# Optimization experiments

Measured on AMD Instinct MI355X. Metric: run time of the kernel, lower is better.

The kernel has to match this reference:

```python
import jax, jax.numpy as jnp
import numpy as np

N, E, C = 50000, 300000, 256  # nodes, edges, hidden size


def setup_inputs() -> dict:
    key = jax.random.key(0)
    ks = jax.random.split(key, 12)
    s = 0.05  # param init scale
    return {
        "x": jax.random.normal(ks[0], (N, C), dtype=jnp.float32),
        "edge_index": jax.random.randint(ks[1], (2, E), 0, N, dtype=jnp.int32),
        # GATConv layer 1 (heads=1): shared lin weight, att_src/att_dst vectors, bias
        "W1": jax.random.normal(ks[2], (C, C), dtype=jnp.float32) * s,
        "a1_src": jax.random.normal(ks[3], (C,), dtype=jnp.float32) * s,
        "a1_dst": jax.random.normal(ks[4], (C,), dtype=jnp.float32) * s,
        "b1": jnp.zeros((C,), dtype=jnp.float32),
        # GATConv layer 2
        "W2": jax.random.normal(ks[5], (C, C), dtype=jnp.float32) * s,
        "a2_src": jax.random.normal(ks[6], (C,), dtype=jnp.float32) * s,
        "a2_dst": jax.random.normal(ks[7], (C,), dtype=jnp.float32) * s,
        "b2": jnp.zeros((C,), dtype=jnp.float32),
        # Final Linear (torch convention: W [out, in], y = x @ W.T + b)
        "Wl": jax.random.normal(ks[8], (C, C), dtype=jnp.float32) * s,
        "bl": jnp.zeros((C,), dtype=jnp.float32),
    }


def _gat_conv(x, src, dst, W, a_src, a_dst, b):
    # PyG GATConv, heads=1, negative_slope=0.2, self-loops already appended.
    h = x @ W                                  # [N, C]
    alpha_src = h @ a_src                      # [N]
    alpha_dst = h @ a_dst                      # [N]
    e = jax.nn.leaky_relu(alpha_src[src] + alpha_dst[dst], 0.2)   # [E']
    # numerically stable softmax over incoming edges of each destination node
    m = jax.ops.segment_max(e, dst, num_segments=N)               # [N]
    ex = jnp.exp(e - m[dst])
    den = jax.ops.segment_sum(ex, dst, num_segments=N)            # [N]
    w = ex / den[dst]                                              # [E']
    out = jax.ops.segment_sum(h[src] * w[:, None], dst, num_segments=N)  # [N, C]
    return out + b


def reference(x, edge_index, W1, a1_src, a1_dst, b1, W2, a2_src, a2_dst, b2, Wl, bl):
    # add_self_loops (done inside each GATConv in PyG; appending once to the
    # input edge list is equivalent since both convs see the same edges)
    loops = jnp.arange(N, dtype=edge_index.dtype)
    ei = jnp.concatenate([edge_index, jnp.stack([loops, loops])], axis=1)
    src, dst = ei[0], ei[1]
    x = jax.nn.relu(_gat_conv(x, src, dst, W1, a1_src, a1_dst, b1))
    x = jax.nn.relu(_gat_conv(x, src, dst, W2, a2_src, a2_dst, b2))
    return x @ Wl.T + bl
```

## Files before the change

kernel.cpp:

```cpp
#include <hip/hip_runtime.h>

#define NN 50000
#define EE 300000
#define ET (EE + NN)
#define CD 256
#define PAD_M 50176
#define NB 196

typedef unsigned short ushortT;
typedef short bf16x8 __attribute__((ext_vector_type(8)));
typedef float f32x4 __attribute__((ext_vector_type(4)));

__device__ __forceinline__ ushortT f2b(float f) {
    unsigned u = __builtin_bit_cast(unsigned, f);
    unsigned r = (u + 0x7FFFu + ((u >> 16) & 1u)) >> 16;
    return (ushortT)r;
}
__device__ __forceinline__ float b2f(ushortT b) {
    return __builtin_bit_cast(float, ((unsigned)b) << 16);
}


__global__ __launch_bounds__(256) void wvec_kernel(
    const float* __restrict__ W1, const float* __restrict__ a1s,
    const float* __restrict__ a1d, const float* __restrict__ W2,
    const float* __restrict__ a2s, const float* __restrict__ a2d,
    float* __restrict__ w1s, float* __restrict__ w1d,
    float* __restrict__ w2s, float* __restrict__ w2d) {
    int b = blockIdx.x;
    const float* W = (b < 64) ? W1 : W2;
    const float* vs = (b < 64) ? a1s : a2s;
    const float* vd = (b < 64) ? a1d : a2d;
    float* os = (b < 64) ? w1s : w2s;
    float* od = (b < 64) ? w1d : w2d;
    int r = (b & 63) * 4 + (threadIdx.x >> 6);
    int lane = threadIdx.x & 63;
    float4 wv = *(const float4*)(W + (size_t)r * CD + lane * 4);
    float4 s4 = *(const float4*)(vs + lane * 4);
    float4 d4 = *(const float4*)(vd + lane * 4);
    float ss = wv.x * s4.x + wv.y * s4.y + wv.z * s4.z + wv.w * s4.w;
    float dd = wv.x * d4.x + wv.y * d4.y + wv.z * d4.z + wv.w * d4.w;
#pragma unroll
    for (int off = 1; off < 64; off <<= 1) {
        ss += __shfl_xor(ss, off);
        dd += __shfl_xor(dd, off);
    }
    if (lane == 0) {
        os[r] = ss;
        od[r] = dd;
    }
}

#define PREP_X 12500
#define PREP_W1 12564
#define PREP_W2 12628
#define PREP_WL 12692
#define PREP_END 12888

__global__ __launch_bounds__(256) void prep_kernel(
    const float* __restrict__ x, const float* __restrict__ W1,
    const float* __restrict__ W2, const float* __restrict__ Wl,
    ushortT* __restrict__ B0, ushortT* __restrict__ W1t,
    ushortT* __restrict__ W2t, ushortT* __restrict__ Wlt,
    int* __restrict__ deg, const float* __restrict__ w1s,
    const float* __restrict__ w1d, float* __restrict__ as1,
    float* __restrict__ ad1) {
    __shared__ float t[32][33];
    int b = blockIdx.x, tidx = threadIdx.x;
    if (b < PREP_X) {
        int node = b * 4 + (tidx >> 6);
        int lane = tidx & 63;
        float4 v = *(const float4*)(x + (size_t)node * CD + lane * 4);
        ushort4 o;
        o.x = f2b(v.x); o.y = f2b(v.y); o.z = f2b(v.z); o.w = f2b(v.w);
        *(ushort4*)(B0 + (size_t)node * CD + lane * 4) = o;
        float4 s4 = *(const float4*)(w1s + lane * 4);
        float4 d4 = *(const float4*)(w1d + lane * 4);
        float ss = v.x * s4.x + v.y * s4.y + v.z * s4.z + v.w * s4.w;
        float dd = v.x * d4.x + v.y * d4.y + v.z * d4.z + v.w * d4.w;
#pragma unroll
        for (int off = 1; off < 64; off <<= 1) {
            ss += __shfl_xor(ss, off);
            dd += __shfl_xor(dd, off);
        }
        if (lane == 0) {
            as1[node] = ss;
            ad1[node] = dd;
        }
    } else if (b < PREP_W2) {
        const float* W = (b < PREP_W1) ? W1 : W2;
        ushortT* Bt = (b < PREP_W1) ? W1t : W2t;
        int rel = b - ((b < PREP_W1) ? PREP_X : PREP_W1);
        int bx = (rel & 7) * 32;
        int by = (rel >> 3) * 32;
        int xx = tidx & 31, yy = tidx >> 5;
        for (int y = yy; y < 32; y += 8) t[y][xx] = W[(size_t)(bx + y) * CD + by + xx];
        __syncthreads();
        for (int y = yy; y < 32; y += 8)
            Bt[(size_t)(by + y) * CD + bx + xx] = f2b(t[xx][y]);
    } else if (b < PREP_WL) {
        int id = (b - PREP_W2) * 256 + tidx;
        float4 v = *(const float4*)(Wl + (size_t)id * 4);
        ushort4 o;
        o.x = f2b(v.x); o.y = f2b(v.y); o.z = f2b(v.z); o.w = f2b(v.w);
        *(ushort4*)(Wlt + (size_t)id * 4) = o;
    } else {
        int i = (b - PREP_WL) * 256 + tidx;
        if (i < NN) deg[i] = 1;
    }
}


__global__ void count_deg_kernel(const int* __restrict__ ei, int* __restrict__ deg) {
    int i = blockIdx.x * blockDim.x + threadIdx.x;
    if (i < EE) atomicAdd(&deg[ei[EE + i]], 1);
}

__global__ __launch_bounds__(256) void scan_part(const int* __restrict__ deg,
                                                 int* __restrict__ bsum) {
    int i = blockIdx.x * 256 + threadIdx.x;
    int v = (i < NN) ? deg[i] : 0;
#pragma unroll
    for (int off = 32; off > 0; off >>= 1) v += __shfl_down(v, off);
    __shared__ int w[4];
    if ((threadIdx.x & 63) == 0) w[threadIdx.x >> 6] = v;
    __syncthreads();
    if (threadIdx.x == 0) bsum[blockIdx.x] = w[0] + w[1] + w[2] + w[3];
}

__global__ __launch_bounds__(256) void scan_fill(const int* __restrict__ deg,
                                                 const int* __restrict__ bsum,
                                                 int* __restrict__ row_start,
                                                 int* __restrict__ fill_pos) {
    __shared__ int s[256];
    int t = threadIdx.x;
    int bv = (t < NB) ? bsum[t] : 0;
    s[t] = bv;
    __syncthreads();
    for (int off = 1; off < 256; off <<= 1) {
        int x = s[t];
        int y = (t >= off) ? s[t - off] : 0;
        __syncthreads();
        s[t] = x + y;
        __syncthreads();
    }
    int boff = s[blockIdx.x] - bsum[blockIdx.x];
    __syncthreads();
    int i = blockIdx.x * 256 + t;
    int v = (i < NN) ? deg[i] : 0;
    s[t] = v;
    __syncthreads();
    for (int off = 1; off < 256; off <<= 1) {
        int x = s[t];
        int y = (t >= off) ? s[t - off] : 0;
        __syncthreads();
        s[t] = x + y;
        __syncthreads();
    }
    int excl = s[t] - v + boff;
    if (i < NN) {
        row_start[i] = excl;
        fill_pos[i] = excl;
    }
    if (blockIdx.x == 0 && t == 0) row_start[NN] = ET;
}

__global__ void fill_csr_kernel(const int* __restrict__ ei, int* __restrict__ fill_pos,
                                int* __restrict__ srcs) {
    int i = blockIdx.x * blockDim.x + threadIdx.x;
    if (i < EE) {
        int s = ei[i];
        int d = ei[EE + i];
        int p = atomicAdd(&fill_pos[d], 1);
        srcs[p] = s;
    } else if (i < ET) {
        int n = i - EE;
        int p = atomicAdd(&fill_pos[n], 1);
        srcs[p] = n;
    }
}


template <int OUTF32>
__global__ __launch_bounds__(256, 4) void gemm_mfma(const ushortT* __restrict__ A,
                                                    const ushortT* __restrict__ Bt,
                                                    const float* __restrict__ bias,
                                                    float* __restrict__ outF,
                                                    ushortT* __restrict__ outB,
                                                    int M) {
    __shared__ ushortT Bs[64 * 256];
    int tid = threadIdx.x;
    int wave = tid >> 6, lane = tid & 63;
    int wm = wave * 32;
    int id = blockIdx.x;
    int bm = (id >> 2) * 128, bn = (id & 3) * 64;
    int l15 = lane & 15, quad = lane >> 4;

#pragma unroll
    for (int p = 0; p < 8; ++p) {
        int c = p * 256 + tid;
        int slot = c >> 5;
        int piece = c & 31;
        int col = (slot & 15) * 4 + (slot >> 4);
        int spiece = piece ^ (slot & 31);
        const ushortT* gb = Bt + (size_t)(bn + col) * CD + spiece * 8;
        __builtin_amdgcn_global_load_lds(
            (const __attribute__((address_space(1))) void*)gb,
            (__attribute__((address_space(3))) void*)(Bs + (size_t)(p * 256 + wave * 64) * 8),
            16, 0, 0);
    }

    bf16x8 a[2][8];
#pragma unroll
    for (int kk = 0; kk < 8; ++kk)
#pragma unroll
        for (int i = 0; i < 2; ++i)
            a[i][kk] = *(const bf16x8*)(A + (size_t)(bm + wm + i * 16 + l15) * CD + kk * 32 + quad * 8);

    __syncthreads();

    f32x4 acc[2][4] = {};

#pragma unroll
    for (int kk = 0; kk < 8; ++kk) {
        bf16x8 b[4];
        int kc = kk * 4 + quad;
#pragma unroll
        for (int j = 0; j < 4; ++j) {
            int slot = j * 16 + l15;
            b[j] = *(const bf16x8*)(Bs + (size_t)slot * 256 + (size_t)(kc ^ (slot & 31)) * 8);
        }
#pragma unroll
        for (int i = 0; i < 2; ++i)
#pragma unroll
            for (int j = 0; j < 4; ++j)
                acc[i][j] = __builtin_amdgcn_mfma_f32_16x16x32_bf16(a[i][kk], b[j], acc[i][j], 0, 0, 0);
    }

    int colb = bn + l15 * 4;
#pragma unroll
    for (int i = 0; i < 2; ++i) {
#pragma unroll
        for (int r = 0; r < 4; ++r) {
            int row = bm + wm + i * 16 + quad * 4 + r;
            if (OUTF32) {
                if (row < M) {
                    float4 bv = *(const float4*)(bias + colb);
                    float4 v;
                    v.x = acc[i][0][r] + bv.x;
                    v.y = acc[i][1][r] + bv.y;
                    v.z = acc[i][2][r] + bv.z;
                    v.w = acc[i][3][r] + bv.w;
                    *(float4*)(outF + (size_t)row * CD + colb) = v;
                }
            } else {
                ushort4 o;
                o.x = f2b(acc[i][0][r]);
                o.y = f2b(acc[i][1][r]);
                o.z = f2b(acc[i][2][r]);
                o.w = f2b(acc[i][3][r]);
                *(ushort4*)(outB + (size_t)row * CD + colb) = o;
            }
        }
    }
}


__device__ __forceinline__ float lrelu02(float x) { return x > 0.f ? x : 0.2f * x; }

template <int ALPHA2>
__global__ __launch_bounds__(256) void gat_agg(const ushortT* __restrict__ h,
                                               const float* __restrict__ as_,
                                               const float* __restrict__ ad_,
                                               const int* __restrict__ row_start,
                                               const int* __restrict__ srcs,
                                               const float* __restrict__ bias,
                                               ushortT* __restrict__ out,
                                               const float* __restrict__ w2s,
                                               const float* __restrict__ w2d,
                                               float* __restrict__ as_n,
                                               float* __restrict__ ad_n) {
    int node = blockIdx.x * 8 + (threadIdx.x >> 5);
    int hl = threadIdx.x & 31;
    if (node >= NN) return;
    int rs = row_start[node];
    int re = row_start[node + 1];
    int deg = re - rs;
    float adst = ad_[node];

    float acc[8] = {0.f, 0.f, 0.f, 0.f, 0.f, 0.f, 0.f, 0.f};

    int maxdeg = max(deg, __shfl_xor(deg, 32));

    if (maxdeg <= 32) {
        int s_lane = srcs[rs + ((hl < deg) ? hl : 0)];
        float e = (hl < deg) ? lrelu02(as_[s_lane] + adst) : -1e30f;
        float m = e;
#pragma unroll
        for (int off = 1; off < 32; off <<= 1) m = fmaxf(m, __shfl_xor(m, off));
        float ex = (hl < deg) ? __expf(e - m) : 0.f;
        float den = ex;
#pragma unroll
        for (int off = 1; off < 32; off <<= 1) den += __shfl_xor(den, off);
        float wl = ex / den;

        for (int kk = 0; kk < maxdeg; kk += 8) {
            int s[8];
            float w[8];
#pragma unroll
            for (int t = 0; t < 8; ++t) {
                int idx = kk + t;
                int ii = (idx < deg) ? idx : 0;
                int sv = __shfl(s_lane, ii, 32);
                float wv = __shfl(wl, ii, 32);
                s[t] = sv;
                w[t] = (idx < deg) ? wv : 0.f;
            }
            bf16x8 hv[8];
#pragma unroll
            for (int t = 0; t < 8; ++t)
                hv[t] = *(const bf16x8*)(h + (size_t)s[t] * CD + hl * 8);
#pragma unroll
            for (int t = 0; t < 8; ++t) {
#pragma unroll
                for (int c = 0; c < 8; ++c)
                    acc[c] += w[t] * b2f((ushortT)hv[t][c]);
            }
        }
    } else {
        float m = -1e30f;
        for (int k = rs + hl; k < re; k += 32) {
            float e = lrelu02(as_[srcs[k]] + adst);
            m = fmaxf(m, e);
        }
#pragma unroll
        for (int off = 1; off < 32; off <<= 1) m = fmaxf(m, __shfl_xor(m, off));
        float den = 0.f;
        for (int k = rs + hl; k < re; k += 32) {
            float e = lrelu02(as_[srcs[k]] + adst);
            den += __expf(e - m);
        }
#pragma unroll
        for (int off = 1; off < 32; off <<= 1) den += __shfl_xor(den, off);
        float inv_den = 1.f / den;
        for (int k = rs; k < re; ++k) {
            int sv = srcs[k];
            float e = lrelu02(as_[sv] + adst);
            float wv = __expf(e - m) * inv_den;
            bf16x8 hv = *(const bf16x8*)(h + (size_t)sv * CD + hl * 8);
#pragma unroll
            for (int c = 0; c < 8; ++c)
                acc[c] += wv * b2f((ushortT)hv[c]);
        }
    }

    float4 bv0 = *(const float4*)(bias + hl * 8);
    float4 bv1 = *(const float4*)(bias + hl * 8 + 4);
    float r[8];
    r[0] = fmaxf(acc[0] + bv0.x, 0.f);
    r[1] = fmaxf(acc[1] + bv0.y, 0.f);
    r[2] = fmaxf(acc[2] + bv0.z, 0.f);
    r[3] = fmaxf(acc[3] + bv0.w, 0.f);
    r[4] = fmaxf(acc[4] + bv1.x, 0.f);
    r[5] = fmaxf(acc[5] + bv1.y, 0.f);
    r[6] = fmaxf(acc[6] + bv1.z, 0.f);
    r[7] = fmaxf(acc[7] + bv1.w, 0.f);
    bf16x8 o;
#pragma unroll
    for (int c = 0; c < 8; ++c) o[c] = (short)f2b(r[c]);
    *(bf16x8*)(out + (size_t)node * CD + hl * 8) = o;

    if (ALPHA2) {
        float4 s0 = *(const float4*)(w2s + hl * 8);
        float4 s1 = *(const float4*)(w2s + hl * 8 + 4);
        float4 d0 = *(const float4*)(w2d + hl * 8);
        float4 d1 = *(const float4*)(w2d + hl * 8 + 4);
        float ss = r[0] * s0.x + r[1] * s0.y + r[2] * s0.z + r[3] * s0.w +
                   r[4] * s1.x + r[5] * s1.y + r[6] * s1.z + r[7] * s1.w;
        float dd = r[0] * d0.x + r[1] * d0.y + r[2] * d0.z + r[3] * d0.w +
                   r[4] * d1.x + r[5] * d1.y + r[6] * d1.z + r[7] * d1.w;
#pragma unroll
        for (int off = 1; off < 32; off <<= 1) {
            ss += __shfl_xor(ss, off);
            dd += __shfl_xor(dd, off);
        }
        if (hl == 0) {
            as_n[node] = ss;
            ad_n[node] = dd;
        }
    }
}


extern "C" void kernel_launch(void* const* d_in, const int* in_sizes, int n_in,
                              void* d_out, int out_size, void* d_ws, size_t ws_size,
                              hipStream_t stream) {
    const float* x = (const float*)d_in[0];
    const int* ei = (const int*)d_in[1];
    const float* W1 = (const float*)d_in[2];
    const float* a1s = (const float*)d_in[3];
    const float* a1d = (const float*)d_in[4];
    const float* b1 = (const float*)d_in[5];
    const float* W2 = (const float*)d_in[6];
    const float* a2s = (const float*)d_in[7];
    const float* a2d = (const float*)d_in[8];
    const float* b2 = (const float*)d_in[9];
    const float* Wl = (const float*)d_in[10];
    const float* bl = (const float*)d_in[11];
    float* out = (float*)d_out;

    char* w = (char*)d_ws;
    ushortT* B0 = (ushortT*)w; w += (size_t)PAD_M * CD * 2;
    ushortT* B1 = (ushortT*)w; w += (size_t)PAD_M * CD * 2;
    ushortT* B2 = (ushortT*)w; w += (size_t)PAD_M * CD * 2;
    ushortT* W1t = (ushortT*)w; w += (size_t)CD * CD * 2;
    ushortT* W2t = (ushortT*)w; w += (size_t)CD * CD * 2;
    ushortT* Wlt = (ushortT*)w; w += (size_t)CD * CD * 2;
    float* as1 = (float*)w; w += (size_t)NN * 4;
    float* ad1 = (float*)w; w += (size_t)NN * 4;
    float* as2 = (float*)w; w += (size_t)NN * 4;
    float* ad2 = (float*)w; w += (size_t)NN * 4;
    float* w1s = (float*)w; w += CD * 4;
    float* w1d = (float*)w; w += CD * 4;
    float* w2s = (float*)w; w += CD * 4;
    float* w2d = (float*)w; w += CD * 4;
    int* deg = (int*)w; w += (size_t)NN * 4;
    int* fill_pos = (int*)w; w += (size_t)NN * 4;
    int* srcs = (int*)w; w += (size_t)ET * 4;
    int* bsum = (int*)w; w += 1024;
    int* row_start = (int*)w; w += (size_t)(NN + 1) * 4;

    wvec_kernel<<<128, 256, 0, stream>>>(W1, a1s, a1d, W2, a2s, a2d,
                                         w1s, w1d, w2s, w2d);

    prep_kernel<<<PREP_END, 256, 0, stream>>>(x, W1, W2, Wl, B0, W1t, W2t, Wlt,
                                              deg, w1s, w1d, as1, ad1);

    count_deg_kernel<<<(EE + 255) / 256, 256, 0, stream>>>(ei, deg);
    scan_part<<<NB, 256, 0, stream>>>(deg, bsum);
    scan_fill<<<NB, 256, 0, stream>>>(deg, bsum, row_start, fill_pos);
    fill_csr_kernel<<<(ET + 255) / 256, 256, 0, stream>>>(ei, fill_pos, srcs);

    int ggrid = (PAD_M / 128) * 4;
    int nagg_blocks = (NN + 7) / 8;

    gemm_mfma<0><<<ggrid, 256, 0, stream>>>(B0, W1t, nullptr, nullptr, B1, NN);
    gat_agg<1><<<nagg_blocks, 256, 0, stream>>>(B1, as1, ad1, row_start, srcs,
                                                b1, B2, w2s, w2d, as2, ad2);

    gemm_mfma<0><<<ggrid, 256, 0, stream>>>(B2, W2t, nullptr, nullptr, B1, NN);
    gat_agg<0><<<nagg_blocks, 256, 0, stream>>>(B1, as2, ad2, row_start, srcs,
                                                b2, B0, nullptr, nullptr,
                                                nullptr, nullptr);

    gemm_mfma<1><<<ggrid, 256, 0, stream>>>(B0, Wlt, bl, out, nullptr, NN);
}
```

Measured before the change: 290.1 us.

## Fuse fp32-to-bf16 conversion and layer-1 attention logits into first GEMM

The separate prep pass that converted x to bf16 and computed the layer-1 alpha_src/alpha_dst dot products is removed. A new GEMM kernel reads fp32 x directly, converts it to bf16 in registers, and computes the attention logits in the column-block-0 tiles. This avoids writing and re-reading a bf16 copy of x. The cost is that each GEMM tile now reads fp32 A, and since there are four column blocks, x is read four times in fp32. The aggregation kernel also issues the first 8 neighbor row gathers before the softmax reductions so that memory latency overlaps the shuffle math.

After: 297.4 us. 2.5% more time.

```diff
diff --git a/kernel.cpp b/kernel.cpp
--- a/kernel.cpp
+++ b/kernel.cpp
@@ -51,46 +51,22 @@
     }
 }
 
-#define PREP_X 12500
-#define PREP_W1 12564
-#define PREP_W2 12628
-#define PREP_WL 12692
-#define PREP_END 12888
+#define PREP_W1 64
+#define PREP_W2 128
+#define PREP_WL 192
+#define PREP_END 388
 
 __global__ __launch_bounds__(256) void prep_kernel(
-    const float* __restrict__ x, const float* __restrict__ W1,
-    const float* __restrict__ W2, const float* __restrict__ Wl,
-    ushortT* __restrict__ B0, ushortT* __restrict__ W1t,
+    const float* __restrict__ W1, const float* __restrict__ W2,
+    const float* __restrict__ Wl, ushortT* __restrict__ W1t,
     ushortT* __restrict__ W2t, ushortT* __restrict__ Wlt,
-    int* __restrict__ deg, const float* __restrict__ w1s,
-    const float* __restrict__ w1d, float* __restrict__ as1,
-    float* __restrict__ ad1) {
+    int* __restrict__ deg) {
     __shared__ float t[32][33];
     int b = blockIdx.x, tidx = threadIdx.x;
-    if (b < PREP_X) {
-        int node = b * 4 + (tidx >> 6);
-        int lane = tidx & 63;
-        float4 v = *(const float4*)(x + (size_t)node * CD + lane * 4);
-        ushort4 o;
-        o.x = f2b(v.x); o.y = f2b(v.y); o.z = f2b(v.z); o.w = f2b(v.w);
-        *(ushort4*)(B0 + (size_t)node * CD + lane * 4) = o;
-        float4 s4 = *(const float4*)(w1s + lane * 4);
-        float4 d4 = *(const float4*)(w1d + lane * 4);
-        float ss = v.x * s4.x + v.y * s4.y + v.z * s4.z + v.w * s4.w;
-        float dd = v.x * d4.x + v.y * d4.y + v.z * d4.z + v.w * d4.w;
-#pragma unroll
-        for (int off = 1; off < 64; off <<= 1) {
-            ss += __shfl_xor(ss, off);
-            dd += __shfl_xor(dd, off);
-        }
-        if (lane == 0) {
-            as1[node] = ss;
-            ad1[node] = dd;
-        }
-    } else if (b < PREP_W2) {
+    if (b < PREP_W2) {
         const float* W = (b < PREP_W1) ? W1 : W2;
         ushortT* Bt = (b < PREP_W1) ? W1t : W2t;
-        int rel = b - ((b < PREP_W1) ? PREP_X : PREP_W1);
+        int rel = b - ((b < PREP_W1) ? 0 : PREP_W1);
         int bx = (rel & 7) * 32;
         int by = (rel >> 3) * 32;
         int xx = tidx & 31, yy = tidx >> 5;
@@ -266,6 +242,126 @@
 }
 
 
+__global__ __launch_bounds__(256, 2) void gemm_mfma_x(
+    const float* __restrict__ A, const ushortT* __restrict__ Bt,
+    ushortT* __restrict__ outB, const float* __restrict__ w1s,
+    const float* __restrict__ w1d, float* __restrict__ as1,
+    float* __restrict__ ad1) {
+    __shared__ ushortT Bs[64 * 256];
+    int tid = threadIdx.x;
+    int wave = tid >> 6, lane = tid & 63;
+    int wm = wave * 32;
+    int id = blockIdx.x;
+    int bm = (id >> 2) * 128, bn = (id & 3) * 64;
+    int l15 = lane & 15, quad = lane >> 4;
+
+#pragma unroll
+    for (int p = 0; p < 8; ++p) {
+        int c = p * 256 + tid;
+        int slot = c >> 5;
+        int piece = c & 31;
+        int col = (slot & 15) * 4 + (slot >> 4);
+        int spiece = piece ^ (slot & 31);
+        const ushortT* gb = Bt + (size_t)(bn + col) * CD + spiece * 8;
+        __builtin_amdgcn_global_load_lds(
+            (const __attribute__((address_space(1))) void*)gb,
+            (__attribute__((address_space(3))) void*)(Bs + (size_t)(p * 256 + wave * 64) * 8),
+            16, 0, 0);
+    }
+
+    int r0 = bm + wm + l15;
+    int r1 = r0 + 16;
+    const float* A0 = A + (size_t)((r0 < NN) ? r0 : (NN - 1)) * CD;
+    const float* A1 = A + (size_t)((r1 < NN) ? r1 : (NN - 1)) * CD;
+    bool doA = (bn == 0);
+    float ss0 = 0.f, sd0 = 0.f, ss1 = 0.f, sd1 = 0.f;
+
+    bf16x8 a[2][8];
+#pragma unroll
+    for (int kk = 0; kk < 8; ++kk) {
+        int cb = kk * 32 + quad * 8;
+        float4 f00 = *(const float4*)(A0 + cb);
+        float4 f01 = *(const float4*)(A0 + cb + 4);
+        float4 f10 = *(const float4*)(A1 + cb);
+        float4 f11 = *(const float4*)(A1 + cb + 4);
+        bf16x8 v0, v1;
+        v0[0] = (short)f2b(f00.x); v0[1] = (short)f2b(f00.y);
+        v0[2] = (short)f2b(f00.z); v0[3] = (short)f2b(f00.w);
+        v0[4] = (short)f2b(f01.x); v0[5] = (short)f2b(f01.y);
+        v0[6] = (short)f2b(f01.z); v0[7] = (short)f2b(f01.w);
+        v1[0] = (short)f2b(f10.x); v1[1] = (short)f2b(f10.y);
+        v1[2] = (short)f2b(f10.z); v1[3] = (short)f2b(f10.w);
+        v1[4] = (short)f2b(f11.x); v1[5] = (short)f2b(f11.y);
+        v1[6] = (short)f2b(f11.z); v1[7] = (short)f2b(f11.w);
+        a[0][kk] = v0;
+        a[1][kk] = v1;
+        if (doA) {
+            float4 ws0 = *(const float4*)(w1s + cb);
+            float4 ws1 = *(const float4*)(w1s + cb + 4);
+            float4 wd0 = *(const float4*)(w1d + cb);
+            float4 wd1 = *(const float4*)(w1d + cb + 4);
+            ss0 += f00.x * ws0.x + f00.y * ws0.y + f00.z * ws0.z + f00.w * ws0.w +
+                   f01.x * ws1.x + f01.y * ws1.y + f01.z * ws1.z + f01.w * ws1.w;
+            sd0 += f00.x * wd0.x + f00.y * wd0.y + f00.z * wd0.z + f00.w * wd0.w +
+                   f01.x * wd1.x + f01.y * wd1.y + f01.z * wd1.z + f01.w * wd1.w;
+            ss1 += f10.x * ws0.x + f10.y * ws0.y + f10.z * ws0.z + f10.w * ws0.w +
+                   f11.x * ws1.x + f11.y * ws1.y + f11.z * ws1.z + f11.w * ws1.w;
+            sd1 += f10.x * wd0.x + f10.y * wd0.y + f10.z * wd0.z + f10.w * wd0.w +
+                   f11.x * wd1.x + f11.y * wd1.y + f11.z * wd1.z + f11.w * wd1.w;
+        }
+    }
+
+    if (doA) {
+#pragma unroll
+        for (int off = 16; off < 64; off <<= 1) {
+            ss0 += __shfl_xor(ss0, off);
+            sd0 += __shfl_xor(sd0, off);
+            ss1 += __shfl_xor(ss1, off);
+            sd1 += __shfl_xor(sd1, off);
+        }
+        if (lane < 16) {
+            if (r0 < NN) { as1[r0] = ss0; ad1[r0] = sd0; }
+            if (r1 < NN) { as1[r1] = ss1; ad1[r1] = sd1; }
+        }
+    }
+
+    __syncthreads();
+
+    f32x4 acc[2][4] = {};
+
+#pragma unroll
+    for (int kk = 0; kk < 8; ++kk) {
+        bf16x8 b[4];
+        int kc = kk * 4 + quad;
+#pragma unroll
+        for (int j = 0; j < 4; ++j) {
+            int slot = j * 16 + l15;
+            b[j] = *(const bf16x8*)(Bs + (size_t)slot * 256 + (size_t)(kc ^ (slot & 31)) * 8);
+        }
+#pragma unroll
+        for (int i = 0; i < 2; ++i)
+#pragma unroll
+            for (int j = 0; j < 4; ++j)
+                acc[i][j] = __builtin_amdgcn_mfma_f32_16x16x32_bf16(a[i][kk], b[j], acc[i][j], 0, 0, 0);
+    }
+
+    int colb = bn + l15 * 4;
+#pragma unroll
+    for (int i = 0; i < 2; ++i) {
+#pragma unroll
+        for (int r = 0; r < 4; ++r) {
+            int row = bm + wm + i * 16 + quad * 4 + r;
+            ushort4 o;
+            o.x = f2b(acc[i][0][r]);
+            o.y = f2b(acc[i][1][r]);
+            o.z = f2b(acc[i][2][r]);
+            o.w = f2b(acc[i][3][r]);
+            *(ushort4*)(outB + (size_t)row * CD + colb) = o;
+        }
+    }
+}
+
+
 __device__ __forceinline__ float lrelu02(float x) { return x > 0.f ? x : 0.2f * x; }
 
 template <int ALPHA2>
@@ -294,6 +390,15 @@
 
     if (maxdeg <= 32) {
         int s_lane = srcs[rs + ((hl < deg) ? hl : 0)];
+
+        int s0[8];
+#pragma unroll
+        for (int t = 0; t < 8; ++t) s0[t] = __shfl(s_lane, (t < deg) ? t : 0, 32);
+        bf16x8 hv[8];
+#pragma unroll
+        for (int t = 0; t < 8; ++t)
+            hv[t] = *(const bf16x8*)(h + (size_t)s0[t] * CD + hl * 8);
+
         float e = (hl < deg) ? lrelu02(as_[s_lane] + adst) : -1e30f;
         float m = e;
 #pragma unroll
@@ -304,7 +409,16 @@
         for (int off = 1; off < 32; off <<= 1) den += __shfl_xor(den, off);
         float wl = ex / den;
 
-        for (int kk = 0; kk < maxdeg; kk += 8) {
+#pragma unroll
+        for (int t = 0; t < 8; ++t) {
+            float wv = __shfl(wl, t, 32);
+            wv = (t < deg) ? wv : 0.f;
+#pragma unroll
+            for (int c = 0; c < 8; ++c)
+                acc[c] += wv * b2f((ushortT)hv[t][c]);
+        }
+
+        for (int kk = 8; kk < maxdeg; kk += 8) {
             int s[8];
             float w[8];
 #pragma unroll
@@ -316,15 +430,15 @@
                 s[t] = sv;
                 w[t] = (idx < deg) ? wv : 0.f;
             }
-            bf16x8 hv[8];
+            bf16x8 hv2[8];
 #pragma unroll
             for (int t = 0; t < 8; ++t)
-                hv[t] = *(const bf16x8*)(h + (size_t)s[t] * CD + hl * 8);
+                hv2[t] = *(const bf16x8*)(h + (size_t)s[t] * CD + hl * 8);
 #pragma unroll
             for (int t = 0; t < 8; ++t) {
 #pragma unroll
                 for (int c = 0; c < 8; ++c)
-                    acc[c] += w[t] * b2f((ushortT)hv[t][c]);
+                    acc[c] += w[t] * b2f((ushortT)hv2[t][c]);
             }
         }
     } else {
@@ -433,8 +547,7 @@
     wvec_kernel<<<128, 256, 0, stream>>>(W1, a1s, a1d, W2, a2s, a2d,
                                          w1s, w1d, w2s, w2d);
 
-    prep_kernel<<<PREP_END, 256, 0, stream>>>(x, W1, W2, Wl, B0, W1t, W2t, Wlt,
-                                              deg, w1s, w1d, as1, ad1);
+    prep_kernel<<<PREP_END, 256, 0, stream>>>(W1, W2, Wl, W1t, W2t, Wlt, deg);
 
     count_deg_kernel<<<(EE + 255) / 256, 256, 0, stream>>>(ei, deg);
     scan_part<<<NB, 256, 0, stream>>>(deg, bsum);
@@ -444,7 +557,7 @@
     int ggrid = (PAD_M / 128) * 4;
     int nagg_blocks = (NN + 7) / 8;
 
-    gemm_mfma<0><<<ggrid, 256, 0, stream>>>(B0, W1t, nullptr, nullptr, B1, NN);
+    gemm_mfma_x<<<ggrid, 256, 0, stream>>>(x, W1t, B1, w1s, w1d, as1, ad1);
     gat_agg<1><<<nagg_blocks, 256, 0, stream>>>(B1, as1, ad1, row_start, srcs,
                                                 b1, B2, w2s, w2d, as2, ad2);
 
```
